# Kernel tuning notes

Measured on AMD Instinct MI355X. Metric: run time of the kernel, lower is better.

## Reference

```python
import jax, jax.numpy as jnp
import numpy as np

B, T, D = 8, 16, 1024
N, K, H = 16, 8, 128   # q heads, kv heads, head dim
S = 8192               # cache size
CUR = 4096             # tokens already in cache
ROPE_THETA = 1000000
EPS = 1e-6
LARGE_NEGATIVE = jnp.finfo(jnp.bfloat16).min


def setup_inputs() -> dict:
    key = jax.random.key(0)
    ks = jax.random.split(key, 8)
    w = 0.02  # realistic weight scale
    return {
        "x": jax.random.normal(ks[0], (B, T, D), jnp.float32),
        "Wq": jax.random.normal(ks[1], (D, N, H), jnp.float32) * w,
        "Wk": jax.random.normal(ks[2], (D, K, H), jnp.float32) * w,
        "Wv": jax.random.normal(ks[3], (D, K, H), jnp.float32) * w,
        "Wo": jax.random.normal(ks[4], (N, H, D), jnp.float32) * w,
        "q_scale": jnp.ones((H,), jnp.float32),
        "k_scale": jnp.ones((H,), jnp.float32),
        "k_cache": jax.random.normal(ks[5], (B, S, K, H), jnp.float32),
        "v_cache": jax.random.normal(ks[6], (B, S, K, H), jnp.float32),
        "segment_ids": jnp.ones((B, T), jnp.int32),
        "start_ind": jnp.zeros((B,), jnp.int32),  # already resolved (= left_pads)
        "cur_ind": CUR,
    }


def _rmsnorm(x, scale, eps=EPS):
    xf = x.astype(jnp.float32)
    y = xf * jax.lax.rsqrt(jnp.mean(xf * xf, axis=-1, keepdims=True) + eps)
    return (y * scale).astype(x.dtype)


def _rope_sincos(positions, head_dim):
    frac = jnp.arange(0, head_dim, 2, dtype=jnp.float32) / head_dim
    inv_freq = 1.0 / (ROPE_THETA ** frac)
    ang = jnp.einsum("BT,k->BTk", positions.astype(jnp.float32), inv_freq,
                     precision=jax.lax.Precision.HIGHEST)
    return jnp.sin(ang), jnp.cos(ang)


def _apply_rope(x, sin, cos):
    x1, x2 = x[..., : x.shape[-1] // 2], x[..., x.shape[-1] // 2 :]
    sin, cos = sin[:, :, None, :], cos[:, :, None, :]
    return jnp.concatenate([x1 * cos - x2 * sin, x2 * cos + x1 * sin], axis=-1).astype(x.dtype)


def reference(x, Wq, Wk, Wv, Wo, q_scale, k_scale, k_cache, v_cache,
              segment_ids, start_ind, cur_ind):
    b, t, _ = x.shape
    n_rep = N // K
    scale = H ** -0.5

    # projections + per-head RMSNorm on q/k
    q = _rmsnorm(jnp.einsum("BTD,DNH->BTNH", x, Wq), q_scale)
    k = _rmsnorm(jnp.einsum("BSD,DKH->BSKH", x, Wk), k_scale)
    v = jnp.einsum("BSD,DKH->BSKH", x, Wv)

    # start index: resolved from left pads on first call
    left_pads = jnp.sum(jnp.cumsum(segment_ids != 0, axis=-1) == 0, -1).astype(jnp.int32)
    start = jnp.where(start_ind < 0, left_pads, start_ind)

    # positions from segment ids, offset by cache cursor
    rel = jax.vmap(lambda row: jnp.where(row != 0, jnp.arange(t) - jnp.argmax(row), 2 ** 30))(segment_ids)
    pos = rel + cur_ind
    sin, cos = _rope_sincos(pos, H)
    q = _apply_rope(q, sin, cos)
    k = _apply_rope(k, sin, cos)

    # KV cache append
    kc = jax.lax.dynamic_update_slice(k_cache, k, (0, cur_ind, 0, 0))
    vc = jax.lax.dynamic_update_slice(v_cache, v, (0, cur_ind, 0, 0))

    # GQA attention against full cache
    qg = q.reshape((b, t, K, n_rep, H))
    logits = jnp.einsum("BTKGH,BSKH->BTSKG", qg, kc) * scale

    q_pos = cur_ind + jnp.arange(t, dtype=jnp.int32)[None, :] - start[:, None]
    ts = jnp.arange(S, dtype=jnp.int32)
    kv_seg = (ts[None, :] >= start[:, None]) & (ts[None, :] < cur_ind + t)
    k_pos = ts[None, :] - start[:, None]
    causal = k_pos[:, None, :] <= q_pos[:, :, None]
    seg_mask = kv_seg[:, None, :] == segment_ids[:, :, None]
    mask = (causal & seg_mask)[:, :, :, None, None]

    logits = jnp.where(mask, logits, LARGE_NEGATIVE)
    w = jax.nn.softmax(logits.astype(jnp.float32), axis=2).astype(logits.dtype)
    o = jnp.einsum("BTSKG,BSKH->BTKGH", w, vc).reshape((b, t, N, H))
    return jnp.einsum("BTNH,NHD->BTD", o, Wo)
```

## Files before the change

kernel.cpp:

```cpp
#include <hip/hip_runtime.h>

#define BB 8
#define TT 16
#define DD 1024
#define NN 16
#define KHN 8
#define HH 128
#define SS 8192
#define NPART 16

typedef __attribute__((ext_vector_type(8))) short bf16x8;
typedef __attribute__((ext_vector_type(4))) float f32x4;

__device__ __forceinline__ unsigned short f2bf(float f) {
  unsigned u = __builtin_bit_cast(unsigned, f);
  u += 0x7FFFu + ((u >> 16) & 1u);
  return (unsigned short)(u >> 16);
}
__device__ __forceinline__ float bf2f(unsigned short h) {
  unsigned u = ((unsigned)h) << 16;
  return __builtin_bit_cast(float, u);
}
__device__ __forceinline__ f32x4 mfma16(bf16x8 a, bf16x8 b, f32x4 c) {
  return __builtin_amdgcn_mfma_f32_16x16x32_bf16(a, b, c, 0, 0, 0);
}
__device__ __forceinline__ void pack4(unsigned short* dst, float a, float b, float c, float d) {
  unsigned lo = (unsigned)f2bf(a) | ((unsigned)f2bf(b) << 16);
  unsigned hi = (unsigned)f2bf(c) | ((unsigned)f2bf(d) << 16);
  *(uint2*)dst = make_uint2(lo, hi);
}

__global__ __launch_bounds__(256) void k_wtrans(
    const float* __restrict__ Wq, const float* __restrict__ Wk,
    const float* __restrict__ Wv, const float* __restrict__ Wo,
    unsigned short* __restrict__ Wt1, unsigned short* __restrict__ Wt2) {
  __shared__ __align__(16) unsigned short Tl[64][66];
  const int tid = threadIdx.x;
  const int z = blockIdx.z;
  const float* src; int K, N; unsigned short* dst;
  if (z == 0)      { src = Wq; K = 1024; N = 2048; dst = Wt1; }
  else if (z == 1) { src = Wk; K = 1024; N = 1024; dst = Wt1 + (size_t)2048 * 1024; }
  else if (z == 2) { src = Wv; K = 1024; N = 1024; dst = Wt1 + (size_t)3072 * 1024; }
  else             { src = Wo; K = 2048; N = 1024; dst = Wt2; }
  const int n0 = blockIdx.x * 64, k0 = blockIdx.y * 64;
  if (n0 >= N || k0 >= K) return;
  {
    const int r = tid >> 4, c4 = (tid & 15) << 2;
#pragma unroll
    for (int p = 0; p < 4; ++p) {
      const int k = p * 16 + r;
      float4 f = *(const float4*)(src + (size_t)(k0 + k) * N + n0 + c4);
      pack4(&Tl[k][c4], f.x, f.y, f.z, f.w);
    }
  }
  __syncthreads();
  {
    const int c8 = tid & 7, nb = tid >> 3;
#pragma unroll
    for (int p = 0; p < 2; ++p) {
      const int n = p * 32 + nb;
      unsigned short tmp[8];
#pragma unroll
      for (int j = 0; j < 8; ++j) tmp[j] = Tl[c8 * 8 + j][n];
      unsigned short* dp = dst + (size_t)(n0 + n) * K + k0 + c8 * 8;
      *(uint4*)dp = *(const uint4*)&tmp[0];
    }
  }
}

__global__ __launch_bounds__(256) void k_qkv_gemm(
    const float* __restrict__ x, const unsigned short* __restrict__ Wt1,
    float* __restrict__ qkv) {
  const int tid = threadIdx.x, lane = tid & 63, wv = tid >> 6;
  const int cc = lane & 15, g = lane >> 4;
  const int m0 = blockIdx.x * 32, n0 = blockIdx.y * 128;
  const int rt = wv >> 1, cb0 = (wv & 1) * 64;
  const int m = m0 + rt * 16 + cc;
  f32x4 acc[4];
#pragma unroll
  for (int i = 0; i < 4; ++i) acc[i] = (f32x4)0.0f;

#pragma unroll 4
  for (int k0 = 0; k0 < 1024; k0 += 32) {
    float4 fa = *(const float4*)(x + (size_t)m * 1024 + k0 + g * 8);
    float4 fb = *(const float4*)(x + (size_t)m * 1024 + k0 + g * 8 + 4);
    bf16x8 af;
    af[0] = (short)f2bf(fa.x); af[1] = (short)f2bf(fa.y);
    af[2] = (short)f2bf(fa.z); af[3] = (short)f2bf(fa.w);
    af[4] = (short)f2bf(fb.x); af[5] = (short)f2bf(fb.y);
    af[6] = (short)f2bf(fb.z); af[7] = (short)f2bf(fb.w);
#pragma unroll
    for (int ct = 0; ct < 4; ++ct) {
      const int n = n0 + cb0 + ct * 16 + cc;
      bf16x8 bf = *(const bf16x8*)(Wt1 + (size_t)n * 1024 + k0 + g * 8);
      acc[ct] = mfma16(af, bf, acc[ct]);
    }
  }
#pragma unroll
  for (int ct = 0; ct < 4; ++ct)
#pragma unroll
    for (int r = 0; r < 4; ++r) {
      int row = m0 + rt * 16 + g * 4 + r;
      int col = n0 + cb0 + ct * 16 + cc;
      qkv[(size_t)row * 4096 + col] = acc[ct][r];
    }
}

__global__ __launch_bounds__(128) void k_normrope(
    const float* __restrict__ qkv, const float* __restrict__ qs,
    const float* __restrict__ ks, const int* __restrict__ seg,
    const int* __restrict__ cur_p,
    unsigned short* __restrict__ qa, unsigned short* __restrict__ ka,
    unsigned short* __restrict__ va) {
  __shared__ float lv[128];
  __shared__ float red[2];
  const int row = blockIdx.x, b = row >> 4, t = row & 15;
  const int hid = blockIdx.y;
  const int h = threadIdx.x;
  float val;
  if (hid < 16)      val = qkv[row * 4096 + hid * 128 + h];
  else if (hid < 24) val = qkv[row * 4096 + 2048 + (hid - 16) * 128 + h];
  else               val = qkv[row * 4096 + 3072 + (hid - 24) * 128 + h];

  if (hid >= 24) {
    int kh = hid - 24;
    va[((b * KHN + kh) * TT + t) * 128 + h] = f2bf(val);
    return;
  }
  float ss = val * val;
#pragma unroll
  for (int m = 1; m < 64; m <<= 1) ss += __shfl_xor(ss, m, 64);
  int wid = threadIdx.x >> 6, lane = threadIdx.x & 63;
  if (lane == 0) red[wid] = ss;
  __syncthreads();
  float mean = (red[0] + red[1]) * (1.0f / 128.0f);
  float scl = (hid < 16) ? qs[h] : ks[h];
  float nrm = val * (1.0f / sqrtf(mean + 1e-6f)) * scl;
  lv[h] = nrm;
  __syncthreads();
  float prt = lv[h ^ 64];
  const int cur = cur_p[0];
  int first = TT;
#pragma unroll
  for (int i = TT - 1; i >= 0; --i)
    if (seg[b * TT + i] != 0) first = i;
  float posf;
  if (seg[b * TT + t] != 0) posf = (float)(t - first + cur);
  else                      posf = (float)(1073741824 + cur);
  int j = h & 63;
  float inv = powf(1.0e6f, -((float)j) * (1.0f / 64.0f));
  float ang = posf * inv;
  float sn = sinf(ang), cs = cosf(ang);
  float outv = (h < 64) ? (nrm * cs - prt * sn) : (nrm * cs + prt * sn);
  if (hid < 16) {
    int kh = hid >> 1, gq = hid & 1;
    qa[((b * KHN + kh) * 32 + gq * 16 + t) * 128 + h] =
        f2bf(outv * 0.08838834764831845f);
  } else {
    int kh = hid - 16;
    ka[((b * KHN + kh) * TT + t) * 128 + h] = f2bf(outv);
  }
}

__global__ __launch_bounds__(256, 2) void k_attn(
    const float* __restrict__ kcache, const float* __restrict__ vcache,
    const unsigned short* __restrict__ qa, const unsigned short* __restrict__ ka,
    const unsigned short* __restrict__ va, const int* __restrict__ seg,
    const int* __restrict__ sind, const int* __restrict__ cur_p,
    float* __restrict__ partO, float* __restrict__ partML) {
  __shared__ __align__(16) unsigned short Kl[4][32][132];
  __shared__ __align__(16) unsigned short Pl[4][32][40];
  __shared__ float mls[2][32][2];
  const int tid = threadIdx.x, wv = tid >> 6, lane = tid & 63;
  const int cc = lane & 15, g = lane >> 4;
  const int pair = blockIdx.x, b = pair >> 3, kh = pair & 7;
  const int qi = blockIdx.y;
  const int cur = cur_p[0];
  const int len = cur + TT;
  int start_b = sind[b];
  if (start_b < 0) {
    int first = TT;
#pragma unroll
    for (int i = TT - 1; i >= 0; --i)
      if (seg[b * TT + i] != 0) first = i;
    start_b = first;
  }
  const int NTt = (len + 31) >> 5;
  const int L = (NTt + NPART - 1) / NPART;
  const int tlo = qi * L;
  const int thi = (tlo + L < NTt) ? (tlo + L) : NTt;

  bf16x8 qf[2][4];
  {
    const unsigned short* qb = qa + ((size_t)pair * 32) * 128;
#pragma unroll
    for (int rb = 0; rb < 2; ++rb)
#pragma unroll
      for (int kk = 0; kk < 4; ++kk)
        qf[rb][kk] = *(const bf16x8*)(qb + (rb * 16 + cc) * 128 + kk * 32 + g * 8);
  }
  const float* kcb = kcache + (size_t)b * (SS * 1024) + kh * 128;
  const float* vcb = vcache + (size_t)b * (SS * 1024) + kh * 128;
  const unsigned short* knb = ka + (size_t)(b * KHN + kh) * (TT * 128);
  const unsigned short* vnb = va + (size_t)(b * KHN + kh) * (TT * 128);

  f32x4 acc[2][8];
  float mreg[2][4], lreg[2][4];
#pragma unroll
  for (int rb = 0; rb < 2; ++rb) {
#pragma unroll
    for (int hb = 0; hb < 8; ++hb) acc[rb][hb] = (f32x4)0.0f;
#pragma unroll
    for (int r = 0; r < 4; ++r) { mreg[rb][r] = -1e30f; lreg[rb][r] = 0.0f; }
  }

  for (int tile = tlo + wv; tile < thi; tile += 4) {
    const int ts0 = tile << 5;
    __builtin_amdgcn_wave_barrier();
    if (ts0 + 32 <= cur) {
#pragma unroll
      for (int i = 0; i < 16; ++i) {
        int ch = lane + (i << 6);
        int r = ch >> 5, c4 = (ch & 31) << 2;
        float4 f = *(const float4*)(kcb + (size_t)(ts0 + r) * 1024 + c4);
        pack4(&Kl[wv][r][c4], f.x, f.y, f.z, f.w);
      }
    } else {
#pragma unroll
      for (int i = 0; i < 16; ++i) {
        int ch = lane + (i << 6);
        int r = ch >> 5, c4 = (ch & 31) << 2;
        int ts = ts0 + r;
        if (ts < cur) {
          float4 f = *(const float4*)(kcb + (size_t)ts * 1024 + c4);
          pack4(&Kl[wv][r][c4], f.x, f.y, f.z, f.w);
        } else {
          int tr = ts - cur; if (tr > TT - 1) tr = TT - 1;
          ushort4 u = *(const ushort4*)(knb + tr * 128 + c4);
          *(ushort4*)&Kl[wv][r][c4] = u;
        }
      }
    }
    __builtin_amdgcn_wave_barrier();
    f32x4 s[2][2];
#pragma unroll
    for (int rb = 0; rb < 2; ++rb)
#pragma unroll
      for (int cb = 0; cb < 2; ++cb) s[rb][cb] = (f32x4)0.0f;
#pragma unroll
    for (int kk = 0; kk < 4; ++kk) {
#pragma unroll
      for (int cb = 0; cb < 2; ++cb) {
        const unsigned short* kp = &Kl[wv][cb * 16 + cc][kk * 32 + g * 8];
        uint2 lo = *(const uint2*)kp;
        uint2 hi = *(const uint2*)(kp + 4);
        bf16x8 kf = __builtin_bit_cast(bf16x8, make_uint4(lo.x, lo.y, hi.x, hi.y));
        s[0][cb] = mfma16(qf[0][kk], kf, s[0][cb]);
        s[1][cb] = mfma16(qf[1][kk], kf, s[1][cb]);
      }
    }
    __builtin_amdgcn_wave_barrier();
    if (ts0 + 32 <= cur) {
#pragma unroll
      for (int i = 0; i < 16; ++i) {
        int ch = lane + (i << 6);
        int r = ch >> 5, c4 = (ch & 31) << 2;
        float4 f = *(const float4*)(vcb + (size_t)(ts0 + r) * 1024 + c4);
        pack4(&Kl[wv][r][c4], f.x, f.y, f.z, f.w);
      }
    } else {
#pragma unroll
      for (int i = 0; i < 16; ++i) {
        int ch = lane + (i << 6);
        int r = ch >> 5, c4 = (ch & 31) << 2;
        int ts = ts0 + r;
        if (ts < cur) {
          float4 f = *(const float4*)(vcb + (size_t)ts * 1024 + c4);
          pack4(&Kl[wv][r][c4], f.x, f.y, f.z, f.w);
        } else {
          int tr = ts - cur; if (tr > TT - 1) tr = TT - 1;
          ushort4 u = *(const ushort4*)(vnb + tr * 128 + c4);
          *(ushort4*)&Kl[wv][r][c4] = u;
        }
      }
    }
    __builtin_amdgcn_wave_barrier();
    float al[2][4];
#pragma unroll
    for (int rb = 0; rb < 2; ++rb) {
#pragma unroll
      for (int r = 0; r < 4; ++r) {
        const int tq = g * 4 + r;
#pragma unroll
        for (int cb = 0; cb < 2; ++cb) {
          int ts = ts0 + cb * 16 + cc;
          bool ok = (ts >= start_b) && (ts <= cur + tq);
          if (!ok) s[rb][cb][r] = -1e30f;
        }
        float tm = fmaxf(s[rb][0][r], s[rb][1][r]);
#pragma unroll
        for (int m = 1; m < 16; m <<= 1) tm = fmaxf(tm, __shfl_xor(tm, m, 64));
        float mn = fmaxf(mreg[rb][r], tm);
        float a = __expf(mreg[rb][r] - mn);
        float p0 = (s[rb][0][r] < -1e29f) ? 0.0f : __expf(s[rb][0][r] - mn);
        float p1 = (s[rb][1][r] < -1e29f) ? 0.0f : __expf(s[rb][1][r] - mn);
        s[rb][0][r] = p0; s[rb][1][r] = p1;
        float rs = p0 + p1;
#pragma unroll
        for (int m = 1; m < 16; m <<= 1) rs += __shfl_xor(rs, m, 64);
        lreg[rb][r] = lreg[rb][r] * a + rs;
        mreg[rb][r] = mn;
        al[rb][r] = a;
      }
    }
#pragma unroll
    for (int rb = 0; rb < 2; ++rb)
#pragma unroll
      for (int cb = 0; cb < 2; ++cb)
#pragma unroll
        for (int r = 0; r < 4; ++r)
          Pl[wv][rb * 16 + g * 4 + r][cb * 16 + cc] = f2bf(s[rb][cb][r]);
    __builtin_amdgcn_wave_barrier();
    bf16x8 pf[2];
#pragma unroll
    for (int rb = 0; rb < 2; ++rb)
      pf[rb] = *(const bf16x8*)&Pl[wv][rb * 16 + cc][g * 8];
    bf16x8 vf[8];
#pragma unroll
    for (int hb = 0; hb < 8; ++hb) {
      int hc = hb * 16 + cc;
#pragma unroll
      for (int j = 0; j < 8; ++j)
        vf[hb][j] = (short)Kl[wv][g * 8 + j][hc];
    }
#pragma unroll
    for (int rb = 0; rb < 2; ++rb)
#pragma unroll
      for (int hb = 0; hb < 8; ++hb) {
        f32x4 t = acc[rb][hb];
#pragma unroll
        for (int r = 0; r < 4; ++r) t[r] *= al[rb][r];
        acc[rb][hb] = mfma16(pf[rb], vf[hb], t);
      }
  }

  float* Oscr = (float*)&Kl[0][0][0];
  auto dump = [&](int sid) {
#pragma unroll
    for (int rb = 0; rb < 2; ++rb)
#pragma unroll
      for (int hb = 0; hb < 8; ++hb)
#pragma unroll
        for (int r = 0; r < 4; ++r)
          Oscr[(sid * 32 + rb * 16 + g * 4 + r) * 128 + hb * 16 + cc] = acc[rb][hb][r];
    if (cc == 0) {
#pragma unroll
      for (int rb = 0; rb < 2; ++rb)
#pragma unroll
        for (int r = 0; r < 4; ++r) {
          mls[sid][rb * 16 + g * 4 + r][0] = mreg[rb][r];
          mls[sid][rb * 16 + g * 4 + r][1] = lreg[rb][r];
        }
    }
  };
  auto mergefrom = [&](int sid) {
    float a0s[2][4], a1s[2][4];
#pragma unroll
    for (int rb = 0; rb < 2; ++rb)
#pragma unroll
      for (int r = 0; r < 4; ++r) {
        int row = rb * 16 + g * 4 + r;
        float mp = mls[sid][row][0], lp = mls[sid][row][1];
        float M = fmaxf(mreg[rb][r], mp);
        float a0 = __expf(mreg[rb][r] - M), a1 = __expf(mp - M);
        lreg[rb][r] = lreg[rb][r] * a0 + lp * a1;
        mreg[rb][r] = M;
        a0s[rb][r] = a0; a1s[rb][r] = a1;
      }
#pragma unroll
    for (int rb = 0; rb < 2; ++rb)
#pragma unroll
      for (int hb = 0; hb < 8; ++hb)
#pragma unroll
        for (int r = 0; r < 4; ++r) {
          int row = rb * 16 + g * 4 + r;
          acc[rb][hb][r] = acc[rb][hb][r] * a0s[rb][r] +
                           Oscr[(sid * 32 + row) * 128 + hb * 16 + cc] * a1s[rb][r];
        }
  };
  __syncthreads();
  if (wv >= 2) dump(wv - 2);
  __syncthreads();
  if (wv < 2) mergefrom(wv);
  __syncthreads();
  if (wv == 1) dump(0);
  __syncthreads();
  if (wv == 0) {
    mergefrom(0);
    size_t pidx = (size_t)pair * NPART + qi;
#pragma unroll
    for (int rb = 0; rb < 2; ++rb)
#pragma unroll
      for (int hb = 0; hb < 8; ++hb)
#pragma unroll
        for (int r = 0; r < 4; ++r)
          partO[(pidx * 32 + rb * 16 + g * 4 + r) * 128 + hb * 16 + cc] = acc[rb][hb][r];
    if (cc == 0) {
#pragma unroll
      for (int rb = 0; rb < 2; ++rb)
#pragma unroll
        for (int r = 0; r < 4; ++r) {
          partML[pidx * 64 + (rb * 16 + g * 4 + r) * 2 + 0] = mreg[rb][r];
          partML[pidx * 64 + (rb * 16 + g * 4 + r) * 2 + 1] = lreg[rb][r];
        }
    }
  }
}

__global__ __launch_bounds__(256) void k_combine(
    const float* __restrict__ partO, const float* __restrict__ partML,
    unsigned short* __restrict__ obf) {
  __shared__ float sc[NPART][32];
  const int pair = blockIdx.x, b = pair >> 3, kh = pair & 7;
  const int isub = blockIdx.y;
  const int tid = threadIdx.x;
  if (tid < 32) {
    float mm[NPART], ll[NPART];
    float M = -3.0e38f;
#pragma unroll
    for (int p = 0; p < NPART; ++p) {
      mm[p] = partML[((size_t)pair * NPART + p) * 64 + tid * 2 + 0];
      ll[p] = partML[((size_t)pair * NPART + p) * 64 + tid * 2 + 1];
      M = fmaxf(M, mm[p]);
    }
    float denom = 0.0f;
#pragma unroll
    for (int p = 0; p < NPART; ++p) denom += __expf(mm[p] - M) * ll[p];
    float inv = (denom > 0.0f) ? 1.0f / denom : 0.0f;
#pragma unroll
    for (int p = 0; p < NPART; ++p) sc[p][tid] = __expf(mm[p] - M) * inv;
  }
  __syncthreads();
#pragma unroll
  for (int i = 0; i < 4; ++i) {
    int idx = tid + ((isub * 4 + i) << 8);
    int row = idx >> 7, hc = idx & 127;
    float o = 0.0f;
#pragma unroll
    for (int p = 0; p < NPART; ++p)
      o += partO[(((size_t)pair * NPART + p) * 32 + row) * 128 + hc] * sc[p][row];
    int gq = row >> 4, t = row & 15, n = kh * 2 + gq;
    obf[((b * TT + t) * NN + n) * 128 + hc] = f2bf(o);
  }
}

__global__ __launch_bounds__(256) void k_out_gemm(
    const unsigned short* __restrict__ obf, const unsigned short* __restrict__ Wt2,
    float* __restrict__ out) {
  const int tid = threadIdx.x, lane = tid & 63, wv = tid >> 6;
  const int cc = lane & 15, g = lane >> 4;
  const int m0 = blockIdx.x * 32, n0 = blockIdx.y * 64;
  const int rt = wv >> 1, cb0 = (wv & 1) * 32;
  const int m = m0 + rt * 16 + cc;
  f32x4 acc[2];
#pragma unroll
  for (int i = 0; i < 2; ++i) acc[i] = (f32x4)0.0f;

#pragma unroll 4
  for (int k0 = 0; k0 < 2048; k0 += 32) {
    bf16x8 af = *(const bf16x8*)(obf + (size_t)m * 2048 + k0 + g * 8);
#pragma unroll
    for (int ct = 0; ct < 2; ++ct) {
      const int d = n0 + cb0 + ct * 16 + cc;
      bf16x8 bf = *(const bf16x8*)(Wt2 + (size_t)d * 2048 + k0 + g * 8);
      acc[ct] = mfma16(af, bf, acc[ct]);
    }
  }
#pragma unroll
  for (int ct = 0; ct < 2; ++ct)
#pragma unroll
    for (int r = 0; r < 4; ++r)
      out[(size_t)(m0 + rt * 16 + g * 4 + r) * 1024 + n0 + cb0 + ct * 16 + cc] = acc[ct][r];
}

extern "C" void kernel_launch(void* const* d_in, const int* in_sizes, int n_in,
                              void* d_out, int out_size, void* d_ws, size_t ws_size,
                              hipStream_t stream) {
  (void)in_sizes; (void)n_in; (void)out_size; (void)ws_size;
  const float* x   = (const float*)d_in[0];
  const float* Wq  = (const float*)d_in[1];
  const float* Wk  = (const float*)d_in[2];
  const float* Wv  = (const float*)d_in[3];
  const float* Wo  = (const float*)d_in[4];
  const float* qs  = (const float*)d_in[5];
  const float* ks  = (const float*)d_in[6];
  const float* kc  = (const float*)d_in[7];
  const float* vc  = (const float*)d_in[8];
  const int* seg   = (const int*)d_in[9];
  const int* sind  = (const int*)d_in[10];
  const int* curp  = (const int*)d_in[11];
  float* out = (float*)d_out;

  char* ws = (char*)d_ws;
  float*          qkv    = (float*)(ws + 0);
  unsigned short* qa     = (unsigned short*)(ws + 2097152);
  unsigned short* ka     = (unsigned short*)(ws + 2621440);
  unsigned short* va     = (unsigned short*)(ws + 2883584);
  float*          partO  = (float*)(ws + 3145728);
  float*          partML = (float*)(ws + 19922944);
  unsigned short* obf    = (unsigned short*)(ws + 20185088);
  unsigned short* Wt1    = (unsigned short*)(ws + 20709376);
  unsigned short* Wt2    = (unsigned short*)(ws + 29097984);

  k_wtrans<<<dim3(32, 32, 4), 256, 0, stream>>>(Wq, Wk, Wv, Wo, Wt1, Wt2);
  k_qkv_gemm<<<dim3(4, 32), 256, 0, stream>>>(x, Wt1, qkv);
  k_normrope<<<dim3(128, 32), 128, 0, stream>>>(qkv, qs, ks, seg, curp, qa, ka, va);
  k_attn<<<dim3(64, NPART), 256, 0, stream>>>(kc, vc, qa, ka, va, seg, sind, curp, partO, partML);
  k_combine<<<dim3(64, 4), 256, 0, stream>>>(partO, partML, obf);
  k_out_gemm<<<dim3(4, 16), 256, 0, stream>>>(obf, Wt2, out);
}
```

Baseline: 153.9 us.

## Load K/V straight into MFMA fragments with next-tile K prefetch in registers

The attention loop no longer stages K and V tiles through LDS. K for the next tile is loaded directly into registers in MFMA operand layout and prefetched while the current tile is processed. V is gathered straight from global memory into registers. Q fragments move to LDS to free registers for the prefetch buffers, and launch bounds drop to one block per CU. This trades LDS round-trips and wave barriers for lower occupancy, scalar strided V loads and higher register pressure.

```diff
diff --git a/kernel.cpp b/kernel.cpp
--- a/kernel.cpp
+++ b/kernel.cpp
@@ -28,6 +28,14 @@
   unsigned lo = (unsigned)f2bf(a) | ((unsigned)f2bf(b) << 16);
   unsigned hi = (unsigned)f2bf(c) | ((unsigned)f2bf(d) << 16);
   *(uint2*)dst = make_uint2(lo, hi);
+}
+__device__ __forceinline__ bf16x8 cvt8(const float4& lo, const float4& hi) {
+  bf16x8 r;
+  r[0] = (short)f2bf(lo.x); r[1] = (short)f2bf(lo.y);
+  r[2] = (short)f2bf(lo.z); r[3] = (short)f2bf(lo.w);
+  r[4] = (short)f2bf(hi.x); r[5] = (short)f2bf(hi.y);
+  r[6] = (short)f2bf(hi.z); r[7] = (short)f2bf(hi.w);
+  return r;
 }
 
 __global__ __launch_bounds__(256) void k_wtrans(
@@ -84,11 +92,7 @@
   for (int k0 = 0; k0 < 1024; k0 += 32) {
     float4 fa = *(const float4*)(x + (size_t)m * 1024 + k0 + g * 8);
     float4 fb = *(const float4*)(x + (size_t)m * 1024 + k0 + g * 8 + 4);
-    bf16x8 af;
-    af[0] = (short)f2bf(fa.x); af[1] = (short)f2bf(fa.y);
-    af[2] = (short)f2bf(fa.z); af[3] = (short)f2bf(fa.w);
-    af[4] = (short)f2bf(fb.x); af[5] = (short)f2bf(fb.y);
-    af[6] = (short)f2bf(fb.z); af[7] = (short)f2bf(fb.w);
+    bf16x8 af = cvt8(fa, fb);
 #pragma unroll
     for (int ct = 0; ct < 4; ++ct) {
       const int n = n0 + cb0 + ct * 16 + cc;
@@ -162,13 +166,13 @@
   }
 }
 
-__global__ __launch_bounds__(256, 2) void k_attn(
+__global__ __launch_bounds__(256, 1) void k_attn(
     const float* __restrict__ kcache, const float* __restrict__ vcache,
     const unsigned short* __restrict__ qa, const unsigned short* __restrict__ ka,
     const unsigned short* __restrict__ va, const int* __restrict__ seg,
     const int* __restrict__ sind, const int* __restrict__ cur_p,
     float* __restrict__ partO, float* __restrict__ partML) {
-  __shared__ __align__(16) unsigned short Kl[4][32][132];
+  __shared__ __align__(16) unsigned short Ql[4][32][132];
   __shared__ __align__(16) unsigned short Pl[4][32][40];
   __shared__ float mls[2][32][2];
   const int tid = threadIdx.x, wv = tid >> 6, lane = tid & 63;
@@ -190,15 +194,19 @@
   const int tlo = qi * L;
   const int thi = (tlo + L < NTt) ? (tlo + L) : NTt;
 
-  bf16x8 qf[2][4];
   {
     const unsigned short* qb = qa + ((size_t)pair * 32) * 128;
 #pragma unroll
-    for (int rb = 0; rb < 2; ++rb)
-#pragma unroll
-      for (int kk = 0; kk < 4; ++kk)
-        qf[rb][kk] = *(const bf16x8*)(qb + (rb * 16 + cc) * 128 + kk * 32 + g * 8);
-  }
+    for (int i = 0; i < 8; ++i) {
+      int ch = i * 64 + lane;
+      int r = ch >> 4, c8 = (ch & 15) << 3;
+      uint4 v = *(const uint4*)(qb + r * 128 + c8);
+      *(uint2*)&Ql[wv][r][c8] = make_uint2(v.x, v.y);
+      *(uint2*)&Ql[wv][r][c8 + 4] = make_uint2(v.z, v.w);
+    }
+  }
+  __builtin_amdgcn_wave_barrier();
+
   const float* kcb = kcache + (size_t)b * (SS * 1024) + kh * 128;
   const float* vcb = vcache + (size_t)b * (SS * 1024) + kh * 128;
   const unsigned short* knb = ka + (size_t)(b * KHN + kh) * (TT * 128);
@@ -214,137 +222,158 @@
     for (int r = 0; r < 4; ++r) { mreg[rb][r] = -1e30f; lreg[rb][r] = 0.0f; }
   }
 
-  for (int tile = tlo + wv; tile < thi; tile += 4) {
+  float4 kraw[16];
+  auto issueK = [&](int tile) {
     const int ts0 = tile << 5;
-    __builtin_amdgcn_wave_barrier();
     if (ts0 + 32 <= cur) {
 #pragma unroll
-      for (int i = 0; i < 16; ++i) {
-        int ch = lane + (i << 6);
-        int r = ch >> 5, c4 = (ch & 31) << 2;
-        float4 f = *(const float4*)(kcb + (size_t)(ts0 + r) * 1024 + c4);
-        pack4(&Kl[wv][r][c4], f.x, f.y, f.z, f.w);
+      for (int kk = 0; kk < 4; ++kk)
+#pragma unroll
+        for (int cb = 0; cb < 2; ++cb) {
+          const float* p = kcb + (size_t)(ts0 + cb * 16 + cc) * 1024 + kk * 32 + g * 8;
+          kraw[kk * 4 + cb * 2 + 0] = *(const float4*)p;
+          kraw[kk * 4 + cb * 2 + 1] = *(const float4*)(p + 4);
+        }
+    } else {
+#pragma unroll
+      for (int kk = 0; kk < 4; ++kk)
+#pragma unroll
+        for (int cb = 0; cb < 2; ++cb) {
+          const int ts = ts0 + cb * 16 + cc;
+          const int idx = kk * 4 + cb * 2;
+          if (ts < cur) {
+            const float* p = kcb + (size_t)ts * 1024 + kk * 32 + g * 8;
+            kraw[idx] = *(const float4*)p;
+            kraw[idx + 1] = *(const float4*)(p + 4);
+          } else {
+            int tr = ts - cur; if (tr > TT - 1) tr = TT - 1;
+            float4 u = *(const float4*)(knb + (size_t)tr * 128 + kk * 32 + g * 8);
+            kraw[idx] = u;
+            kraw[idx + 1] = u;
+          }
+        }
+    }
+  };
+
+  {
+    const int t0 = tlo + wv;
+    if (t0 < thi) issueK(t0);
+    for (int tile = t0; tile < thi; tile += 4) {
+      const int ts0 = tile << 5;
+      const bool fast = (ts0 + 32 <= cur);
+
+      f32x4 s[2][2];
+#pragma unroll
+      for (int rb = 0; rb < 2; ++rb)
+#pragma unroll
+        for (int cb = 0; cb < 2; ++cb) s[rb][cb] = (f32x4)0.0f;
+#pragma unroll
+      for (int kk = 0; kk < 4; ++kk) {
+        const unsigned short* q0 = &Ql[wv][cc][kk * 32 + g * 8];
+        const unsigned short* q1 = &Ql[wv][16 + cc][kk * 32 + g * 8];
+        uint2 a0 = *(const uint2*)q0, a1 = *(const uint2*)(q0 + 4);
+        bf16x8 qf0 = __builtin_bit_cast(bf16x8, make_uint4(a0.x, a0.y, a1.x, a1.y));
+        uint2 b0 = *(const uint2*)q1, b1 = *(const uint2*)(q1 + 4);
+        bf16x8 qf1 = __builtin_bit_cast(bf16x8, make_uint4(b0.x, b0.y, b1.x, b1.y));
+#pragma unroll
+        for (int cb = 0; cb < 2; ++cb) {
+          const int idx = kk * 4 + cb * 2;
+          bf16x8 kf;
+          if (fast) {
+            kf = cvt8(kraw[idx], kraw[idx + 1]);
+          } else {
+            const int ts = ts0 + cb * 16 + cc;
+            if (ts < cur) kf = cvt8(kraw[idx], kraw[idx + 1]);
+            else          kf = __builtin_bit_cast(bf16x8, kraw[idx]);
+          }
+          s[0][cb] = mfma16(qf0, kf, s[0][cb]);
+          s[1][cb] = mfma16(qf1, kf, s[1][cb]);
+        }
       }
-    } else {
-#pragma unroll
-      for (int i = 0; i < 16; ++i) {
-        int ch = lane + (i << 6);
-        int r = ch >> 5, c4 = (ch & 31) << 2;
-        int ts = ts0 + r;
-        if (ts < cur) {
-          float4 f = *(const float4*)(kcb + (size_t)ts * 1024 + c4);
-          pack4(&Kl[wv][r][c4], f.x, f.y, f.z, f.w);
-        } else {
-          int tr = ts - cur; if (tr > TT - 1) tr = TT - 1;
-          ushort4 u = *(const ushort4*)(knb + tr * 128 + c4);
-          *(ushort4*)&Kl[wv][r][c4] = u;
+
+      float vraw[8][8];
+      if (fast) {
+#pragma unroll
+        for (int hb = 0; hb < 8; ++hb) {
+          const int hc = hb * 16 + cc;
+#pragma unroll
+          for (int j = 0; j < 8; ++j)
+            vraw[hb][j] = vcb[(size_t)(ts0 + g * 8 + j) * 1024 + hc];
+        }
+      } else {
+#pragma unroll
+        for (int hb = 0; hb < 8; ++hb) {
+          const int hc = hb * 16 + cc;
+#pragma unroll
+          for (int j = 0; j < 8; ++j) {
+            const int ts = ts0 + g * 8 + j;
+            if (ts < cur) vraw[hb][j] = vcb[(size_t)ts * 1024 + hc];
+            else { int tr = ts - cur; if (tr > TT - 1) tr = TT - 1; vraw[hb][j] = bf2f(vnb[tr * 128 + hc]); }
+          }
         }
       }
-    }
-    __builtin_amdgcn_wave_barrier();
-    f32x4 s[2][2];
-#pragma unroll
-    for (int rb = 0; rb < 2; ++rb)
-#pragma unroll
-      for (int cb = 0; cb < 2; ++cb) s[rb][cb] = (f32x4)0.0f;
-#pragma unroll
-    for (int kk = 0; kk < 4; ++kk) {
-#pragma unroll
-      for (int cb = 0; cb < 2; ++cb) {
-        const unsigned short* kp = &Kl[wv][cb * 16 + cc][kk * 32 + g * 8];
-        uint2 lo = *(const uint2*)kp;
-        uint2 hi = *(const uint2*)(kp + 4);
-        bf16x8 kf = __builtin_bit_cast(bf16x8, make_uint4(lo.x, lo.y, hi.x, hi.y));
-        s[0][cb] = mfma16(qf[0][kk], kf, s[0][cb]);
-        s[1][cb] = mfma16(qf[1][kk], kf, s[1][cb]);
+      if (tile + 4 < thi) issueK(tile + 4);
+      __builtin_amdgcn_sched_barrier(0);
+
+      float al[2][4];
+#pragma unroll
+      for (int rb = 0; rb < 2; ++rb) {
+#pragma unroll
+        for (int r = 0; r < 4; ++r) {
+          const int tq = g * 4 + r;
+#pragma unroll
+          for (int cb = 0; cb < 2; ++cb) {
+            int ts = ts0 + cb * 16 + cc;
+            bool ok = (ts >= start_b) && (ts <= cur + tq);
+            if (!ok) s[rb][cb][r] = -1e30f;
+          }
+          float tm = fmaxf(s[rb][0][r], s[rb][1][r]);
+#pragma unroll
+          for (int m = 1; m < 16; m <<= 1) tm = fmaxf(tm, __shfl_xor(tm, m, 64));
+          float mn = fmaxf(mreg[rb][r], tm);
+          float a = __expf(mreg[rb][r] - mn);
+          float p0 = (s[rb][0][r] < -1e29f) ? 0.0f : __expf(s[rb][0][r] - mn);
+          float p1 = (s[rb][1][r] < -1e29f) ? 0.0f : __expf(s[rb][1][r] - mn);
+          s[rb][0][r] = p0; s[rb][1][r] = p1;
+          float rs = p0 + p1;
+#pragma unroll
+          for (int m = 1; m < 16; m <<= 1) rs += __shfl_xor(rs, m, 64);
+          lreg[rb][r] = lreg[rb][r] * a + rs;
+          mreg[rb][r] = mn;
+          al[rb][r] = a;
+        }
       }
-    }
-    __builtin_amdgcn_wave_barrier();
-    if (ts0 + 32 <= cur) {
-#pragma unroll
-      for (int i = 0; i < 16; ++i) {
-        int ch = lane + (i << 6);
-        int r = ch >> 5, c4 = (ch & 31) << 2;
-        float4 f = *(const float4*)(vcb + (size_t)(ts0 + r) * 1024 + c4);
-        pack4(&Kl[wv][r][c4], f.x, f.y, f.z, f.w);
-      }
-    } else {
-#pragma unroll
-      for (int i = 0; i < 16; ++i) {
-        int ch = lane + (i << 6);
-        int r = ch >> 5, c4 = (ch & 31) << 2;
-        int ts = ts0 + r;
-        if (ts < cur) {
-          float4 f = *(const float4*)(vcb + (size_t)ts * 1024 + c4);
-          pack4(&Kl[wv][r][c4], f.x, f.y, f.z, f.w);
-        } else {
-          int tr = ts - cur; if (tr > TT - 1) tr = TT - 1;
-          ushort4 u = *(const ushort4*)(vnb + tr * 128 + c4);
-          *(ushort4*)&Kl[wv][r][c4] = u;
-        }
-      }
-    }
-    __builtin_amdgcn_wave_barrier();
-    float al[2][4];
-#pragma unroll
-    for (int rb = 0; rb < 2; ++rb) {
-#pragma unroll
-      for (int r = 0; r < 4; ++r) {
-        const int tq = g * 4 + r;
-#pragma unroll
-        for (int cb = 0; cb < 2; ++cb) {
-          int ts = ts0 + cb * 16 + cc;
-          bool ok = (ts >= start_b) && (ts <= cur + tq);
-          if (!ok) s[rb][cb][r] = -1e30f;
-        }
-        float tm = fmaxf(s[rb][0][r], s[rb][1][r]);
-#pragma unroll
-        for (int m = 1; m < 16; m <<= 1) tm = fmaxf(tm, __shfl_xor(tm, m, 64));
-        float mn = fmaxf(mreg[rb][r], tm);
-        float a = __expf(mreg[rb][r] - mn);
-        float p0 = (s[rb][0][r] < -1e29f) ? 0.0f : __expf(s[rb][0][r] - mn);
-        float p1 = (s[rb][1][r] < -1e29f) ? 0.0f : __expf(s[rb][1][r] - mn);
-        s[rb][0][r] = p0; s[rb][1][r] = p1;
-        float rs = p0 + p1;
-#pragma unroll
-        for (int m = 1; m < 16; m <<= 1) rs += __shfl_xor(rs, m, 64);
-        lreg[rb][r] = lreg[rb][r] * a + rs;
-        mreg[rb][r] = mn;
-        al[rb][r] = a;
-      }
-    }
-#pragma unroll
-    for (int rb = 0; rb < 2; ++rb)
-#pragma unroll
-      for (int cb = 0; cb < 2; ++cb)
-#pragma unroll
-        for (int r = 0; r < 4; ++r)
-          Pl[wv][rb * 16 + g * 4 + r][cb * 16 + cc] = f2bf(s[rb][cb][r]);
-    __builtin_amdgcn_wave_barrier();
-    bf16x8 pf[2];
-#pragma unroll
-    for (int rb = 0; rb < 2; ++rb)
-      pf[rb] = *(const bf16x8*)&Pl[wv][rb * 16 + cc][g * 8];
-    bf16x8 vf[8];
-#pragma unroll
-    for (int hb = 0; hb < 8; ++hb) {
-      int hc = hb * 16 + cc;
-#pragma unroll
-      for (int j = 0; j < 8; ++j)
-        vf[hb][j] = (short)Kl[wv][g * 8 + j][hc];
-    }
-#pragma unroll
-    for (int rb = 0; rb < 2; ++rb)
-#pragma unroll
-      for (int hb = 0; hb < 8; ++hb) {
-        f32x4 t = acc[rb][hb];
-#pragma unroll
-        for (int r = 0; r < 4; ++r) t[r] *= al[rb][r];
-        acc[rb][hb] = mfma16(pf[rb], vf[hb], t);
-      }
-  }
-
-  float* Oscr = (float*)&Kl[0][0][0];
+#pragma unroll
+      for (int rb = 0; rb < 2; ++rb)
+#pragma unroll
+        for (int cb = 0; cb < 2; ++cb)
+#pragma unroll
+          for (int r = 0; r < 4; ++r)
+            Pl[wv][rb * 16 + g * 4 + r][cb * 16 + cc] = f2bf(s[rb][cb][r]);
+      __builtin_amdgcn_wave_barrier();
+      bf16x8 pf[2];
+#pragma unroll
+      for (int rb = 0; rb < 2; ++rb)
+        pf[rb] = *(const bf16x8*)&Pl[wv][rb * 16 + cc][g * 8];
+      bf16x8 vf[8];
+#pragma unroll
+      for (int hb = 0; hb < 8; ++hb)
+#pragma unroll
+        for (int j = 0; j < 8; ++j)
+          vf[hb][j] = (short)f2bf(vraw[hb][j]);
+#pragma unroll
+      for (int rb = 0; rb < 2; ++rb)
+#pragma unroll
+        for (int hb = 0; hb < 8; ++hb) {
+          f32x4 t = acc[rb][hb];
+#pragma unroll
+          for (int r = 0; r < 4; ++r) t[r] *= al[rb][r];
+          acc[rb][hb] = mfma16(pf[rb], vf[hb], t);
+        }
+    }
+  }
+
+  float* Oscr = (float*)&Ql[0][0][0];
   auto dump = [&](int sid) {
 #pragma unroll
     for (int rb = 0; rb < 2; ++rb)
```

Result: slower. 176.6 us (+14.7%).

## Load V directly into MFMA registers, drop P LDS buffer, use packed bf16 convert

Applied to the files above, without the earlier changes.

The attention kernel now loads V-cache values from global memory straight into the per-lane B-operand registers (scalar, strided loads per element), instead of staging V in LDS and then reading it back transposed. The softmax probabilities reuse the K LDS tile instead of a separate buffer, and the occupancy hint is raised to 3 blocks per SIMD. f32-to-bf16 conversion now uses the hardware packed convert instruction. The aim is to cut LDS round-trips and shared-memory footprint, at the cost of uncoalesced 4-byte global loads for V and more register pressure under the tighter launch bound.

```diff
diff --git a/kernel.cpp b/kernel.cpp
--- a/kernel.cpp
+++ b/kernel.cpp
@@ -24,10 +24,18 @@
 __device__ __forceinline__ f32x4 mfma16(bf16x8 a, bf16x8 b, f32x4 c) {
   return __builtin_amdgcn_mfma_f32_16x16x32_bf16(a, b, c, 0, 0, 0);
 }
+__device__ __forceinline__ unsigned cvt_pair(float a, float b) {
+  unsigned r;
+  asm("v_cvt_pk_bf16_f32 %0, %1, %2" : "=v"(r) : "v"(a), "v"(b));
+  return r;
+}
 __device__ __forceinline__ void pack4(unsigned short* dst, float a, float b, float c, float d) {
-  unsigned lo = (unsigned)f2bf(a) | ((unsigned)f2bf(b) << 16);
-  unsigned hi = (unsigned)f2bf(c) | ((unsigned)f2bf(d) << 16);
-  *(uint2*)dst = make_uint2(lo, hi);
+  *(uint2*)dst = make_uint2(cvt_pair(a, b), cvt_pair(c, d));
+}
+__device__ __forceinline__ bf16x8 cvt8(const float4& lo, const float4& hi) {
+  return __builtin_bit_cast(bf16x8,
+      make_uint4(cvt_pair(lo.x, lo.y), cvt_pair(lo.z, lo.w),
+                 cvt_pair(hi.x, hi.y), cvt_pair(hi.z, hi.w)));
 }
 
 __global__ __launch_bounds__(256) void k_wtrans(
@@ -84,11 +92,7 @@
   for (int k0 = 0; k0 < 1024; k0 += 32) {
     float4 fa = *(const float4*)(x + (size_t)m * 1024 + k0 + g * 8);
     float4 fb = *(const float4*)(x + (size_t)m * 1024 + k0 + g * 8 + 4);
-    bf16x8 af;
-    af[0] = (short)f2bf(fa.x); af[1] = (short)f2bf(fa.y);
-    af[2] = (short)f2bf(fa.z); af[3] = (short)f2bf(fa.w);
-    af[4] = (short)f2bf(fb.x); af[5] = (short)f2bf(fb.y);
-    af[6] = (short)f2bf(fb.z); af[7] = (short)f2bf(fb.w);
+    bf16x8 af = cvt8(fa, fb);
 #pragma unroll
     for (int ct = 0; ct < 4; ++ct) {
       const int n = n0 + cb0 + ct * 16 + cc;
@@ -162,14 +166,13 @@
   }
 }
 
-__global__ __launch_bounds__(256, 2) void k_attn(
+__global__ __launch_bounds__(256, 3) void k_attn(
     const float* __restrict__ kcache, const float* __restrict__ vcache,
     const unsigned short* __restrict__ qa, const unsigned short* __restrict__ ka,
     const unsigned short* __restrict__ va, const int* __restrict__ seg,
     const int* __restrict__ sind, const int* __restrict__ cur_p,
     float* __restrict__ partO, float* __restrict__ partML) {
   __shared__ __align__(16) unsigned short Kl[4][32][132];
-  __shared__ __align__(16) unsigned short Pl[4][32][40];
   __shared__ float mls[2][32][2];
   const int tid = threadIdx.x, wv = tid >> 6, lane = tid & 63;
   const int cc = lane & 15, g = lane >> 4;
@@ -259,32 +262,39 @@
         s[1][cb] = mfma16(qf[1][kk], kf, s[1][cb]);
       }
     }
-    __builtin_amdgcn_wave_barrier();
+    bf16x8 vf[8];
     if (ts0 + 32 <= cur) {
 #pragma unroll
-      for (int i = 0; i < 16; ++i) {
-        int ch = lane + (i << 6);
-        int r = ch >> 5, c4 = (ch & 31) << 2;
-        float4 f = *(const float4*)(vcb + (size_t)(ts0 + r) * 1024 + c4);
-        pack4(&Kl[wv][r][c4], f.x, f.y, f.z, f.w);
+      for (int hb = 0; hb < 8; ++hb) {
+        const int hc = hb * 16 + cc;
+        float v0 = vcb[(size_t)(ts0 + g * 8 + 0) * 1024 + hc];
+        float v1 = vcb[(size_t)(ts0 + g * 8 + 1) * 1024 + hc];
+        float v2 = vcb[(size_t)(ts0 + g * 8 + 2) * 1024 + hc];
+        float v3 = vcb[(size_t)(ts0 + g * 8 + 3) * 1024 + hc];
+        float v4 = vcb[(size_t)(ts0 + g * 8 + 4) * 1024 + hc];
+        float v5 = vcb[(size_t)(ts0 + g * 8 + 5) * 1024 + hc];
+        float v6 = vcb[(size_t)(ts0 + g * 8 + 6) * 1024 + hc];
+        float v7 = vcb[(size_t)(ts0 + g * 8 + 7) * 1024 + hc];
+        vf[hb] = __builtin_bit_cast(bf16x8,
+            make_uint4(cvt_pair(v0, v1), cvt_pair(v2, v3),
+                       cvt_pair(v4, v5), cvt_pair(v6, v7)));
       }
     } else {
 #pragma unroll
-      for (int i = 0; i < 16; ++i) {
-        int ch = lane + (i << 6);
-        int r = ch >> 5, c4 = (ch & 31) << 2;
-        int ts = ts0 + r;
-        if (ts < cur) {
-          float4 f = *(const float4*)(vcb + (size_t)ts * 1024 + c4);
-          pack4(&Kl[wv][r][c4], f.x, f.y, f.z, f.w);
-        } else {
-          int tr = ts - cur; if (tr > TT - 1) tr = TT - 1;
-          ushort4 u = *(const ushort4*)(vnb + tr * 128 + c4);
-          *(ushort4*)&Kl[wv][r][c4] = u;
+      for (int hb = 0; hb < 8; ++hb) {
+        const int hc = hb * 16 + cc;
+        float vv[8];
+#pragma unroll
+        for (int j = 0; j < 8; ++j) {
+          const int ts = ts0 + g * 8 + j;
+          if (ts < cur) vv[j] = vcb[(size_t)ts * 1024 + hc];
+          else { int tr = ts - cur; if (tr > TT - 1) tr = TT - 1; vv[j] = bf2f(vnb[tr * 128 + hc]); }
         }
-      }
-    }
-    __builtin_amdgcn_wave_barrier();
+        vf[hb] = __builtin_bit_cast(bf16x8,
+            make_uint4(cvt_pair(vv[0], vv[1]), cvt_pair(vv[2], vv[3]),
+                       cvt_pair(vv[4], vv[5]), cvt_pair(vv[6], vv[7])));
+      }
+    }
     float al[2][4];
 #pragma unroll
     for (int rb = 0; rb < 2; ++rb) {
@@ -313,25 +323,22 @@
         al[rb][r] = a;
       }
     }
+    __builtin_amdgcn_wave_barrier();
 #pragma unroll
     for (int rb = 0; rb < 2; ++rb)
 #pragma unroll
       for (int cb = 0; cb < 2; ++cb)
 #pragma unroll
         for (int r = 0; r < 4; ++r)
-          Pl[wv][rb * 16 + g * 4 + r][cb * 16 + cc] = f2bf(s[rb][cb][r]);
+          Kl[wv][rb * 16 + g * 4 + r][cb * 16 + cc] = f2bf(s[rb][cb][r]);
     __builtin_amdgcn_wave_barrier();
     bf16x8 pf[2];
 #pragma unroll
-    for (int rb = 0; rb < 2; ++rb)
-      pf[rb] = *(const bf16x8*)&Pl[wv][rb * 16 + cc][g * 8];
-    bf16x8 vf[8];
-#pragma unroll
-    for (int hb = 0; hb < 8; ++hb) {
-      int hc = hb * 16 + cc;
-#pragma unroll
-      for (int j = 0; j < 8; ++j)
-        vf[hb][j] = (short)Kl[wv][g * 8 + j][hc];
+    for (int rb = 0; rb < 2; ++rb) {
+      const unsigned short* pp = &Kl[wv][rb * 16 + cc][g * 8];
+      uint2 lo = *(const uint2*)pp;
+      uint2 hi = *(const uint2*)(pp + 4);
+      pf[rb] = __builtin_bit_cast(bf16x8, make_uint4(lo.x, lo.y, hi.x, hi.y));
     }
 #pragma unroll
     for (int rb = 0; rb < 2; ++rb)
```

After: 271.3 us. +76.2%, slower.
